# Performance work log

Hardware: AMD Instinct MI355X
Metric: run time of the kernel (lower is better)

Reference implementation:

```python
import jax, jax.numpy as jnp
import numpy as np
from jax import lax

WIN_SIZE = 11
SIGMA = 1.5
WEIGHTS = jnp.array([0.0448, 0.2856, 0.3001, 0.2363, 0.1333], dtype=jnp.float32)
C1 = (0.01 * 1.0) ** 2  # val_range = 1.0
C2 = (0.03 * 1.0) ** 2


def gaussian_kernel2d(kernel_size, sigma):
    g = jnp.arange(kernel_size, dtype=jnp.float32) - kernel_size // 2
    g = jnp.exp(-(g ** 2) / (2.0 * sigma ** 2))
    g = g / g.sum()
    return jnp.outer(g, g)  # [k, k]


def depthwise_conv(x, k2d):
    # x: [B, C, H, W]; same gaussian window applied per-channel (groups=C), VALID padding
    C = x.shape[1]
    w = jnp.broadcast_to(k2d, (C, 1) + k2d.shape).astype(x.dtype)
    return lax.conv_general_dilated(x, w, (1, 1), 'VALID',
                                    feature_group_count=C,
                                    dimension_numbers=('NCHW', 'OIHW', 'NCHW'))


def ssim_index(x, y, k2d, nonnegative=True):
    # returns (ss, cs) each of shape [B, C] (spatial mean, per channel)
    m1 = depthwise_conv(x, k2d)
    m2 = depthwise_conv(y, k2d)
    m12 = m1 * m2
    m1s = m1 * m1
    m2s = m2 * m2
    v1 = depthwise_conv(x * x, k2d) - m1s
    v2 = depthwise_conv(y * y, k2d) - m2s
    cov = depthwise_conv(x * y, k2d) - m12
    cs = (2.0 * cov + C2) / (v1 + v2 + C2)
    ss = (2.0 * m12 + C1) / (m1s + m2s + C1) * cs
    ss = ss.reshape(ss.shape[0], ss.shape[1], -1).mean(axis=-1)
    cs = cs.reshape(cs.shape[0], cs.shape[1], -1).mean(axis=-1)
    if nonnegative:
        ss = jnp.maximum(ss, 0.0)
        cs = jnp.maximum(cs, 0.0)
    return ss, cs


def avg_pool2(x):
    # F.avg_pool2d(kernel_size=2). Input spatial dims are even at every scale
    # (512 -> 32), so ceil_mode never pads; plain 2x2/2 mean pooling is exact.
    s = lax.reduce_window(x, jnp.array(0.0, x.dtype), lax.add,
                          (1, 1, 2, 2), (1, 1, 2, 2), 'VALID')
    return s * 0.25


def setup_inputs() -> dict:
    key = jax.random.key(0)
    k1, k2 = jax.random.split(key)
    B, C, H, W = 4, 12, 512, 512
    pred = jax.random.normal(k1, (B, C, H, W), dtype=jnp.float32)
    target = jax.random.randint(k2, (B, H, W), 0, C, dtype=jnp.int64)
    return {"pred": pred, "target": target}


def reference(pred, target):
    # MS_SSIMLoss.forward with process_input=True, nonnegative=True.
    # The per-class python loop in the original is an independent depthwise
    # computation per channel -> vectorized here as a C-channel grouped conv;
    # loss = mean over classes of (1 - mean over batch of msss) == 1 - mean(msss).
    num_classes = pred.shape[1]
    x = jax.nn.softmax(pred, axis=1)
    y = jax.nn.one_hot(target, num_classes, dtype=pred.dtype).transpose(0, 3, 1, 2)
    k2d = gaussian_kernel2d(WIN_SIZE, SIGMA)
    m = WEIGHTS.shape[0]
    vals = []
    for i in range(m):
        if i > 0:
            x = avg_pool2(x)
            y = avg_pool2(y)
        ss, cs = ssim_index(x, y, k2d, nonnegative=True)
        vals.append(cs if i + 1 < m else ss)
    stacked = jnp.stack(vals, axis=-1)  # [B, C, m]
    msss = jnp.prod(stacked ** WEIGHTS, axis=-1)  # [B, C]
    return 1.0 - msss.mean()
```

## Files before the change

### kernel.cpp

```cpp
#include <hip/hip_runtime.h>

#define NCH 12
#define NB  4
#define BC  48
#define HW0 (512 * 512)

#define GK_INIT { 0.00102840f, 0.00759863f, 0.03600078f, 0.10936081f, \
                  0.21300541f, 0.26601164f, 0.21300541f, 0.10936081f, \
                  0.03600078f, 0.00759863f, 0.00102840f }

__global__ void k_denom(const float4* __restrict__ pred, float4* __restrict__ U,
                        double* __restrict__ acc) {
    if (blockIdx.x == 0) {
        for (int t = threadIdx.x; t < 480; t += 256) acc[t] = 0.0;
    }
    int i = blockIdx.x * blockDim.x + threadIdx.x;
    if (i >= NB * (HW0 / 4)) return;
    int b = i >> 16;
    int p = i & 65535;
    const float4* base = pred + (((size_t)b * NCH) << 16) + p;
    float4 s = make_float4(0.f, 0.f, 0.f, 0.f);
#pragma unroll
    for (int c = 0; c < NCH; ++c) {
        float4 v = base[(size_t)c << 16];
        s.x += expf(v.x); s.y += expf(v.y);
        s.z += expf(v.z); s.w += expf(v.w);
    }
    float4 u;
    u.x = 1.f / s.x; u.y = 1.f / s.y; u.z = 1.f / s.z; u.w = 1.f / s.w;
    U[((size_t)b << 16) + p] = u;
}

__global__ __launch_bounds__(256, 8)
void k_ssim0(const float* __restrict__ pred, const float* __restrict__ U,
             const int* __restrict__ tgt, double* __restrict__ acc,
             float* __restrict__ Xp, unsigned short* __restrict__ Yp) {
    constexpr int SS = 43;
    constexpr int TS = 35;
    constexpr int H = 512, W = 512, OH = 502, OW = 502, tilesX = 16;
    __shared__ float sx[42 * SS + 4];
    __shared__ uint2 tm4[42 * TS];
    __shared__ unsigned long long ybits[30];
    __shared__ float red[8];

    const float gk[11] = GK_INIT;

    const int bc = blockIdx.y;
    const int tile = blockIdx.x;
    const int ty = tile / tilesX, tx = tile - ty * tilesX;
    const int oy = ty * 32, ox = tx * 32;
    const int tid = threadIdx.x;
    const bool interior = (oy + 41 < H) && (ox + 41 < W);

    const int b = bc / NCH, cls = bc - (bc / NCH) * NCH;
    const float* Pb = pred + (((size_t)b * NCH + cls) << 18);
    const float* Ub = U + ((size_t)b << 18);
    const int* Tb = tgt + ((size_t)b << 18);

    {
        int r = tid / 42, c = tid - (tid / 42) * 42;
#pragma unroll
        for (int k = 0; k < 7; ++k) {
            bool inr = (k < 6) || (tid < 228);
            int gy = oy + r, gx = ox + c;
            bool ld = inr && (interior || (gy < H && gx < W));
            float xv = 0.f;
            bool bit = false;
            if (ld) {
                int off = gy * W + gx;
                xv = expf(Pb[off]) * Ub[off];
                bit = (Tb[off] == cls);
            }
            unsigned long long mk = __ballot(bit);
            if ((tid & 63) == 0) ybits[(tid >> 6) + (k << 2)] = mk;
            if (inr) sx[r * SS + c] = xv;
            c += 4; r += 6;
            if (c >= 42) { c -= 42; r += 1; }
        }
        if (tid == 0) { ybits[28] = 0ull; ybits[29] = 0ull; }
    }
    __syncthreads();

    if (tid < 252) {
        int rr = tid / 6, s = tid - (tid / 6) * 6;
        int c0 = s * 6;
        const float* px = sx + rr * SS + c0;
        float ac0[6] = {}, ac1[6] = {}, ac2[6] = {}, ac3[6] = {};
        unsigned long long win;
        {
            int i0 = rr * 42 + c0;
            int w = i0 >> 6, sh = i0 & 63;
            unsigned long long lo = ybits[w], hi = ybits[w + 1];
            win = sh ? ((lo >> sh) | (hi << (64 - sh))) : lo;
        }
#pragma unroll
        for (int j = 0; j < 16; ++j) {
            float xv = px[j];
            float xx = xv * xv;
            bool bit = (win >> j) & 1;
            float yv = bit ? 1.f : 0.f;
            float xy = bit ? xv : 0.f;
#pragma unroll
            for (int o = 0; o < 6; ++o) {
                int kk = j - o;
                if (kk >= 0 && kk <= 10) {
                    float g = gk[kk];
                    ac0[o] = fmaf(g, xv, ac0[o]);
                    ac1[o] = fmaf(g, yv, ac1[o]);
                    ac2[o] = fmaf(g, xx, ac2[o]);
                    ac3[o] = fmaf(g, xy, ac3[o]);
                }
            }
        }
        int ob = rr * TS + c0;
#pragma unroll
        for (int o = 0; o < 6; ++o) {
            if (c0 + o < 32) {
                unsigned ua = __float_as_uint(ac0[o]);
                unsigned ub = __float_as_uint(ac1[o]);
                unsigned uc = __float_as_uint(ac2[o]);
                unsigned ud = __float_as_uint(ac3[o]);
                tm4[ob + o] = make_uint2((ua >> 16) | (ub & 0xFFFF0000u),
                                         (uc >> 16) | (ud & 0xFFFF0000u));
            }
        }
    }
    __syncthreads();

    const float C1 = 1e-4f, C2 = 9e-4f;
    const int cc = tid & 31, rg = tid >> 5, r0 = rg << 2;
    float a0[4] = {}, a1[4] = {}, a2[4] = {}, a3[4] = {};
    const int vb = r0 * TS + cc;
#pragma unroll
    for (int k = 0; k < 14; ++k) {
        uint2 tv = tm4[vb + k * TS];
        float m1v = __uint_as_float(tv.x << 16);
        float m2v = __uint_as_float(tv.x & 0xFFFF0000u);
        float xxv = __uint_as_float(tv.y << 16);
        float xyv = __uint_as_float(tv.y & 0xFFFF0000u);
#pragma unroll
        for (int j = 0; j < 4; ++j) {
            int kk = k - j;
            if (kk >= 0 && kk <= 10) {
                float g = gk[kk];
                a0[j] = fmaf(g, m1v, a0[j]);
                a1[j] = fmaf(g, m2v, a1[j]);
                a2[j] = fmaf(g, xxv, a2[j]);
                a3[j] = fmaf(g, xyv, a3[j]);
            }
        }
    }
    float cs_l = 0.f, ss_l = 0.f;
    const bool colok = (ox + cc < OW);
#pragma unroll
    for (int j = 0; j < 4; ++j) {
        if (colok && (oy + r0 + j < OH)) {
            float m1 = a0[j], m2 = a1[j];
            float sxx = a2[j], sxy_ = a3[j];
            float m11 = m1 * m1, m22 = m2 * m2, m12 = m1 * m2;
            float v1 = sxx - m11, v2 = m2 - m22, cov = sxy_ - m12;
            float d1 = m11 + m22 + C1, d2 = v1 + v2 + C2;
            float n2 = 2.f * cov + C2;
            float q = 1.f / (d1 * d2);
            cs_l = fmaf(n2 * d1, q, cs_l);
            ss_l = fmaf((2.f * m12 + C1) * n2, q, ss_l);
        }
    }

    {
        int py = tid >> 4, pxx = tid & 15;
        int s0 = (py * 2) * SS + pxx * 2;
        float xs = 0.25f * (sx[s0] + sx[s0 + 1] + sx[s0 + SS] + sx[s0 + SS + 1]);
        size_t oidx = ((size_t)bc * 256 + (oy >> 1) + py) * 256 + (ox >> 1) + pxx;
        Xp[oidx] = xs;
        int i0 = (py * 2) * 42 + pxx * 2, i1 = i0 + 42;
        unsigned c0 = (unsigned)((ybits[i0 >> 6] >> (i0 & 63)) & 1ull);
        unsigned c1 = (unsigned)((ybits[(i0 + 1) >> 6] >> ((i0 + 1) & 63)) & 1ull);
        unsigned c2 = (unsigned)((ybits[i1 >> 6] >> (i1 & 63)) & 1ull);
        unsigned c3 = (unsigned)((ybits[(i1 + 1) >> 6] >> ((i1 + 1) & 63)) & 1ull);
        Yp[oidx] = (unsigned short)((c0 + c1 + c2 + c3) << 6);
    }

    for (int off = 32; off; off >>= 1) {
        cs_l += __shfl_down(cs_l, off);
        ss_l += __shfl_down(ss_l, off);
    }
    int wv = tid >> 6, ln = tid & 63;
    if (ln == 0) { red[wv] = cs_l; red[4 + wv] = ss_l; }
    __syncthreads();
    if (tid == 0) {
        double cs_b = (double)red[0] + (double)red[1] + (double)red[2] + (double)red[3];
        double ss_b = (double)red[4] + (double)red[5] + (double)red[6] + (double)red[7];
        atomicAdd(&acc[bc], cs_b);
        atomicAdd(&acc[48 + bc], ss_b);
    }
}

template <int PIN>
__device__ __forceinline__ void ssim_tile_g(
    const float* __restrict__ Xs, const unsigned short* __restrict__ Ys,
    int H, int W, int OH, int OW, int tilesX, int tile, int bc,
    double* __restrict__ acc, int scale,
    float* sx, float4* tm4, float* tm5, unsigned short* syu, float* red) {
    constexpr int SS = 43;
    constexpr int TS = 35;
    const float gk[11] = GK_INIT;

    const int ty = tile / tilesX, tx = tile - ty * tilesX;
    const int oy = ty * 32, ox = tx * 32;
    const int tid = threadIdx.x;
    const bool interior = (oy + 41 < H) && (ox + 41 < W);

    constexpr int SC = 1 << PIN;
    const int SW = W * SC;
    const float* Xb = Xs + (size_t)bc * H * W * SC * SC;
    const unsigned short* Yb = Ys + (size_t)bc * H * W * SC * SC;

    {
        int r = tid / 42, c = tid - (tid / 42) * 42;
#pragma unroll
        for (int k = 0; k < 7; ++k) {
            bool inr = (k < 6) || (tid < 228);
            int gy = oy + r, gx = ox + c;
            bool ld = inr && (interior || (gy < H && gx < W));
            float xv = 0.f;
            unsigned short yv = 0;
            if (ld) {
                if constexpr (PIN == 0) {
                    int off = gy * SW + gx;
                    xv = Xb[off];
                    yv = Yb[off];
                } else {
                    const float* q = Xb + (SC * gy) * SW + SC * gx;
                    const unsigned short* qy = Yb + (SC * gy) * SW + SC * gx;
                    float s = 0.f; unsigned us = 0;
#pragma unroll
                    for (int a = 0; a < SC; ++a) {
#pragma unroll
                        for (int e = 0; e < SC; ++e) {
                            s += q[a * SW + e];
                            us += qy[a * SW + e];
                        }
                    }
                    xv = s * (1.f / (float)(SC * SC));
                    yv = (unsigned short)(us >> (2 * PIN));
                }
            }
            if (inr) { sx[r * SS + c] = xv; syu[r * SS + c] = yv; }
            c += 4; r += 6;
            if (c >= 42) { c -= 42; r += 1; }
        }
    }
    __syncthreads();

    if (tid < 252) {
        int rr = tid / 6, s = tid - (tid / 6) * 6;
        int c0 = s * 6;
        const float* px = sx + rr * SS + c0;
        const unsigned short* pyu = syu + rr * SS + c0;
        float ac0[6] = {}, ac1[6] = {}, ac2[6] = {}, ac3[6] = {}, ac4[6] = {};
#pragma unroll
        for (int j = 0; j < 16; ++j) {
            float xv = px[j];
            float xx = xv * xv;
            float yv = (float)pyu[j];
            float xy = xv * yv;
            float yy = yv * yv;
#pragma unroll
            for (int o = 0; o < 6; ++o) {
                int kk = j - o;
                if (kk >= 0 && kk <= 10) {
                    float g = gk[kk];
                    ac0[o] = fmaf(g, xv, ac0[o]);
                    ac1[o] = fmaf(g, yv, ac1[o]);
                    ac2[o] = fmaf(g, xx, ac2[o]);
                    ac3[o] = fmaf(g, xy, ac3[o]);
                    ac4[o] = fmaf(g, yy, ac4[o]);
                }
            }
        }
        int ob = rr * TS + c0;
#pragma unroll
        for (int o = 0; o < 6; ++o) {
            if (c0 + o < 32) {
                tm4[ob + o] = make_float4(ac0[o], ac1[o], ac2[o], ac3[o]);
                tm5[ob + o] = ac4[o];
            }
        }
    }
    __syncthreads();

    const float C1 = 1e-4f, C2 = 9e-4f;
    const int cc = tid & 31, rg = tid >> 5, r0 = rg << 2;
    float a0[4] = {}, a1[4] = {}, a2[4] = {}, a3[4] = {}, a4[4] = {};
    const int vb = r0 * TS + cc;
#pragma unroll
    for (int k = 0; k < 14; ++k) {
        float4 tv = tm4[vb + k * TS];
        float t4 = tm5[vb + k * TS];
#pragma unroll
        for (int j = 0; j < 4; ++j) {
            int kk = k - j;
            if (kk >= 0 && kk <= 10) {
                float g = gk[kk];
                a0[j] = fmaf(g, tv.x, a0[j]);
                a1[j] = fmaf(g, tv.y, a1[j]);
                a2[j] = fmaf(g, tv.z, a2[j]);
                a3[j] = fmaf(g, tv.w, a3[j]);
                a4[j] = fmaf(g, t4, a4[j]);
            }
        }
    }
    float cs_l = 0.f, ss_l = 0.f;
    const bool colok = (ox + cc < OW);
#pragma unroll
    for (int j = 0; j < 4; ++j) {
        if (colok && (oy + r0 + j < OH)) {
            float m1 = a0[j];
            float m2 = a1[j] * (1.f / 256.f);
            float sxx = a2[j];
            float sxy_ = a3[j] * (1.f / 256.f);
            float syy_ = a4[j] * (1.f / 65536.f);
            float m11 = m1 * m1, m22 = m2 * m2, m12 = m1 * m2;
            float v1 = sxx - m11, v2 = syy_ - m22, cov = sxy_ - m12;
            float d1 = m11 + m22 + C1, d2 = v1 + v2 + C2;
            float n2 = 2.f * cov + C2;
            float q = 1.f / (d1 * d2);
            cs_l = fmaf(n2 * d1, q, cs_l);
            ss_l = fmaf((2.f * m12 + C1) * n2, q, ss_l);
        }
    }

    for (int offs = 32; offs; offs >>= 1) {
        cs_l += __shfl_down(cs_l, offs);
        ss_l += __shfl_down(ss_l, offs);
    }
    int wv = tid >> 6, ln = tid & 63;
    if (ln == 0) { red[wv] = cs_l; red[4 + wv] = ss_l; }
    __syncthreads();
    if (tid == 0) {
        double cs_b = (double)red[0] + (double)red[1] + (double)red[2] + (double)red[3];
        double ss_b = (double)red[4] + (double)red[5] + (double)red[6] + (double)red[7];
        atomicAdd(&acc[scale * 96 + bc], cs_b);
        atomicAdd(&acc[scale * 96 + 48 + bc], ss_b);
    }
}

__global__ __launch_bounds__(256, 4)
void k_rest(const float* __restrict__ X1, const unsigned short* __restrict__ Y1,
            double* __restrict__ acc) {
    __shared__ float sx[42 * 43 + 4];
    __shared__ float4 tm4[42 * 35];
    __shared__ float tm5[42 * 35];
    __shared__ unsigned short syu[42 * 43 + 4];
    __shared__ float red[8];
    const int gb = blockIdx.x;

    if (gb < 3072) {
        ssim_tile_g<0>(X1, Y1, 256, 256, 246, 246, 8, gb & 63, gb >> 6,
                       acc, 1, sx, tm4, tm5, syu, red);
    } else if (gb < 3840) {
        int t = gb - 3072;
        ssim_tile_g<1>(X1, Y1, 128, 128, 118, 118, 4, t & 15, t >> 4,
                       acc, 2, sx, tm4, tm5, syu, red);
    } else if (gb < 4032) {
        int t = gb - 3840;
        ssim_tile_g<2>(X1, Y1, 64, 64, 54, 54, 2, t & 3, t >> 2,
                       acc, 3, sx, tm4, tm5, syu, red);
    } else {
        ssim_tile_g<3>(X1, Y1, 32, 32, 22, 22, 1, 0, gb - 4032,
                       acc, 4, sx, tm4, tm5, syu, red);
    }
}

__global__ void k_final(const double* __restrict__ acc, float* __restrict__ out) {
    const float wts[5] = {0.0448f, 0.2856f, 0.3001f, 0.2363f, 0.1333f};
    const float cnt[5] = {252004.f, 60516.f, 13924.f, 2916.f, 484.f};
    int tid = threadIdx.x;
    float msss = 0.f;
    if (tid < BC) {
        msss = 1.f;
#pragma unroll
        for (int s = 0; s < 5; ++s) {
            double a = (s < 4) ? acc[s * 96 + tid] : acc[s * 96 + 48 + tid];
            float v = fmaxf((float)(a / (double)cnt[s]), 0.f);
            msss *= powf(v, wts[s]);
        }
    }
    for (int off = 32; off; off >>= 1) msss += __shfl_down(msss, off);
    if (tid == 0) out[0] = 1.f - msss * (1.f / (float)BC);
}

extern "C" void kernel_launch(void* const* d_in, const int* in_sizes, int n_in,
                              void* d_out, int out_size, void* d_ws, size_t ws_size,
                              hipStream_t stream) {
    const float* pred = (const float*)d_in[0];
    const int*   tgt  = (const int*)d_in[1];
    float* out = (float*)d_out;

    double* acc = (double*)d_ws;
    float* U  = (float*)(acc + 480);
    float* X1 = U + (size_t)NB * 512 * 512;
    unsigned short* Y1 = (unsigned short*)(X1 + (size_t)BC * 256 * 256);

    k_denom<<<(NB * (HW0 / 4) + 255) / 256, 256, 0, stream>>>(
        (const float4*)pred, (float4*)U, acc);

    k_ssim0<<<dim3(256, BC), 256, 0, stream>>>(pred, U, tgt, acc, X1, Y1);

    k_rest<<<dim3(4080), 256, 0, stream>>>(X1, Y1, acc);

    k_final<<<1, 64, 0, stream>>>(acc, out);
}
```

Before: 250.8 us.

## Store horizontal-pass intermediates as bf16, vectorize pooled loads, reorder block scheduling

The horizontal-convolution intermediates in shared memory are rounded to bf16 and packed into a uint2 plus a ushort instead of float4 plus float. This shrinks LDS per block so launch bounds can rise from 4 to 6 blocks per CU. The multi-scale pooled loads now use float2/float4 and ushort vector reads. Block order in k_rest is reversed so the expensive coarse-scale tiles are scheduled first. The bf16 storage cuts the precision of the means and variances before the vertical pass, which risks accuracy in the variance subtraction.

```diff
diff --git a/kernel.cpp b/kernel.cpp
--- a/kernel.cpp
+++ b/kernel.cpp
@@ -201,7 +201,7 @@
     const float* __restrict__ Xs, const unsigned short* __restrict__ Ys,
     int H, int W, int OH, int OW, int tilesX, int tile, int bc,
     double* __restrict__ acc, int scale,
-    float* sx, float4* tm4, float* tm5, unsigned short* syu, float* red) {
+    float* sx, uint2* tm4, unsigned short* tm5, unsigned short* syu, float* red) {
     constexpr int SS = 43;
     constexpr int TS = 35;
     const float gk[11] = GK_INIT;
@@ -236,10 +236,22 @@
                     float s = 0.f; unsigned us = 0;
 #pragma unroll
                     for (int a = 0; a < SC; ++a) {
-#pragma unroll
-                        for (int e = 0; e < SC; ++e) {
-                            s += q[a * SW + e];
-                            us += qy[a * SW + e];
+                        const float* qr = q + a * SW;
+                        const unsigned short* qyr = qy + a * SW;
+                        if constexpr (PIN == 1) {
+                            float2 f = *(const float2*)qr;
+                            s += f.x + f.y;
+                            ushort2 uy = *(const ushort2*)qyr;
+                            us += (unsigned)uy.x + (unsigned)uy.y;
+                        } else {
+#pragma unroll
+                            for (int e4 = 0; e4 < SC / 4; ++e4) {
+                                float4 f = *(const float4*)(qr + e4 * 4);
+                                s += (f.x + f.y) + (f.z + f.w);
+                                ushort4 uy = *(const ushort4*)(qyr + e4 * 4);
+                                us += ((unsigned)uy.x + (unsigned)uy.y)
+                                    + ((unsigned)uy.z + (unsigned)uy.w);
+                            }
                         }
                     }
                     xv = s * (1.f / (float)(SC * SC));
@@ -283,8 +295,14 @@
 #pragma unroll
         for (int o = 0; o < 6; ++o) {
             if (c0 + o < 32) {
-                tm4[ob + o] = make_float4(ac0[o], ac1[o], ac2[o], ac3[o]);
-                tm5[ob + o] = ac4[o];
+                unsigned ua = __float_as_uint(ac0[o]) + 0x8000u;
+                unsigned ub = __float_as_uint(ac1[o]) + 0x8000u;
+                unsigned uc = __float_as_uint(ac2[o]) + 0x8000u;
+                unsigned ud = __float_as_uint(ac3[o]) + 0x8000u;
+                unsigned ue = __float_as_uint(ac4[o]) + 0x8000u;
+                tm4[ob + o] = make_uint2((ua >> 16) | (ub & 0xFFFF0000u),
+                                         (uc >> 16) | (ud & 0xFFFF0000u));
+                tm5[ob + o] = (unsigned short)(ue >> 16);
             }
         }
     }
@@ -296,17 +314,21 @@
     const int vb = r0 * TS + cc;
 #pragma unroll
     for (int k = 0; k < 14; ++k) {
-        float4 tv = tm4[vb + k * TS];
-        float t4 = tm5[vb + k * TS];
+        uint2 tv = tm4[vb + k * TS];
+        float t0 = __uint_as_float(tv.x << 16);
+        float t1 = __uint_as_float(tv.x & 0xFFFF0000u);
+        float t2 = __uint_as_float(tv.y << 16);
+        float t3 = __uint_as_float(tv.y & 0xFFFF0000u);
+        float t4 = __uint_as_float((unsigned)tm5[vb + k * TS] << 16);
 #pragma unroll
         for (int j = 0; j < 4; ++j) {
             int kk = k - j;
             if (kk >= 0 && kk <= 10) {
                 float g = gk[kk];
-                a0[j] = fmaf(g, tv.x, a0[j]);
-                a1[j] = fmaf(g, tv.y, a1[j]);
-                a2[j] = fmaf(g, tv.z, a2[j]);
-                a3[j] = fmaf(g, tv.w, a3[j]);
+                a0[j] = fmaf(g, t0, a0[j]);
+                a1[j] = fmaf(g, t1, a1[j]);
+                a2[j] = fmaf(g, t2, a2[j]);
+                a3[j] = fmaf(g, t3, a3[j]);
                 a4[j] = fmaf(g, t4, a4[j]);
             }
         }
@@ -346,30 +368,31 @@
     }
 }
 
-__global__ __launch_bounds__(256, 4)
+__global__ __launch_bounds__(256, 6)
 void k_rest(const float* __restrict__ X1, const unsigned short* __restrict__ Y1,
             double* __restrict__ acc) {
     __shared__ float sx[42 * 43 + 4];
-    __shared__ float4 tm4[42 * 35];
-    __shared__ float tm5[42 * 35];
+    __shared__ uint2 tm4[42 * 35];
+    __shared__ unsigned short tm5[42 * 35];
     __shared__ unsigned short syu[42 * 43 + 4];
     __shared__ float red[8];
     const int gb = blockIdx.x;
 
-    if (gb < 3072) {
-        ssim_tile_g<0>(X1, Y1, 256, 256, 246, 246, 8, gb & 63, gb >> 6,
-                       acc, 1, sx, tm4, tm5, syu, red);
-    } else if (gb < 3840) {
-        int t = gb - 3072;
+    if (gb < 48) {
+        ssim_tile_g<3>(X1, Y1, 32, 32, 22, 22, 1, 0, gb,
+                       acc, 4, sx, tm4, tm5, syu, red);
+    } else if (gb < 240) {
+        int t = gb - 48;
+        ssim_tile_g<2>(X1, Y1, 64, 64, 54, 54, 2, t & 3, t >> 2,
+                       acc, 3, sx, tm4, tm5, syu, red);
+    } else if (gb < 1008) {
+        int t = gb - 240;
         ssim_tile_g<1>(X1, Y1, 128, 128, 118, 118, 4, t & 15, t >> 4,
                        acc, 2, sx, tm4, tm5, syu, red);
-    } else if (gb < 4032) {
-        int t = gb - 3840;
-        ssim_tile_g<2>(X1, Y1, 64, 64, 54, 54, 2, t & 3, t >> 2,
-                       acc, 3, sx, tm4, tm5, syu, red);
     } else {
-        ssim_tile_g<3>(X1, Y1, 32, 32, 22, 22, 1, 0, gb - 4032,
-                       acc, 4, sx, tm4, tm5, syu, red);
+        int t = gb - 1008;
+        ssim_tile_g<0>(X1, Y1, 256, 256, 246, 246, 8, t & 63, t >> 6,
+                       acc, 1, sx, tm4, tm5, syu, red);
     }
 }
 
```

New measurement: 252.6 us. No clear change (+0.7%).
